# Optimization experiments

Hardware: AMD Instinct MI355X
Metric: run time of the kernel (lower is better)

## Reference

```python
import jax, jax.numpy as jnp
import numpy as np

C = 768
NUM_HEADS = 12
HEAD_DIM = C // NUM_HEADS
AGENT_NUM = 49
POOL = 7  # sqrt(agent_num)
EPS = 1e-5


def _with_bias_ln(x, w, b):
    # LayerNorm over last dim, biased variance, eps=1e-5
    mu = x.mean(-1, keepdims=True)
    var = ((x - mu) ** 2).mean(-1, keepdims=True)
    return (x - mu) / jnp.sqrt(var + EPS) * w + b


def setup_inputs() -> dict:
    key = jax.random.key(0)
    ks = jax.random.split(key, 8)
    B, H, W = 8, 56, 56
    inp = {
        "x": jax.random.normal(ks[0], (B, C, H, W), dtype=jnp.float32),
        "y": jax.random.normal(ks[1], (B, C, H, W), dtype=jnp.float32),
        "ln1_w": jnp.ones((C,), jnp.float32),
        "ln1_b": jnp.zeros((C,), jnp.float32),
        "ln2_w": jnp.ones((C,), jnp.float32),
        "ln2_b": jnp.zeros((C,), jnp.float32),
        # torch nn.Linear weight layout: [out, in]
        "wq1": jax.random.normal(ks[2], (C, C), jnp.float32) * 0.02,
        "wq2": jax.random.normal(ks[3], (C, C), jnp.float32) * 0.02,
        "wkv": jax.random.normal(ks[4], (2 * C, C), jnp.float32) * 0.02,
        "wproj": jax.random.normal(ks[5], (C, C), jnp.float32) * 0.02,
        "bproj": jnp.zeros((C,), jnp.float32),
    }
    return inp


def reference(x, y, ln1_w, ln1_b, ln2_w, ln2_b, wq1, wq2, wkv, wproj, bproj):
    b, c, h, w = x.shape
    n = h * w
    nh, hd = NUM_HEADS, HEAD_DIM
    scale = hd ** (-0.5)

    # NCHW -> (b, n, c) token layout
    xt = x.reshape(b, c, n).transpose(0, 2, 1)
    yt = y.reshape(b, c, n).transpose(0, 2, 1)

    xt = _with_bias_ln(xt, ln1_w, ln1_b)
    yt = _with_bias_ln(yt, ln2_w, ln2_b)

    q = jnp.einsum('bnc,oc->bno', xt, wq1)        # (b, n, c)
    q_agent = jnp.einsum('bnc,oc->bno', yt, wq2)  # (b, n, c)
    kv = jnp.einsum('bnc,oc->bno', xt, wkv)       # (b, n, 2c)
    k, v = kv[..., :c], kv[..., c:]

    # Adaptive avg pool q_agent to 7x7 agent tokens (56/7 = 8 exact windows)
    qa = q_agent.reshape(b, h, w, c)
    qa = qa.reshape(b, POOL, h // POOL, POOL, w // POOL, c).mean(axis=(2, 4))
    agent_tokens = qa.reshape(b, AGENT_NUM, c)

    # split heads: (b, heads, tokens, head_dim)
    q = q.reshape(b, n, nh, hd).transpose(0, 2, 1, 3)
    k = k.reshape(b, n, nh, hd).transpose(0, 2, 1, 3)
    v = v.reshape(b, n, nh, hd).transpose(0, 2, 1, 3)
    at = agent_tokens.reshape(b, AGENT_NUM, nh, hd).transpose(0, 2, 1, 3)

    # stage 1: agent tokens attend over keys -> pooled values
    agent_attn = jax.nn.softmax(jnp.einsum('bhad,bhnd->bhan', at * scale, k), axis=-1)
    agent_v = jnp.einsum('bhan,bhnd->bhad', agent_attn, v)  # (b, h, A, hd)

    # stage 2: queries attend over agent tokens
    q_attn = jax.nn.softmax(jnp.einsum('bhnd,bhad->bhna', q * scale, at), axis=-1)
    out = jnp.einsum('bhna,bhad->bhnd', q_attn, agent_v)  # (b, h, n, hd)

    out = out.transpose(0, 2, 1, 3).reshape(b, n, c)
    out = jnp.einsum('bnc,oc->bno', out, wproj) + bproj
    return out.transpose(0, 2, 1).reshape(b, c, h, w)
```

## Files before the change

### kernel.cpp

```cpp
#include <hip/hip_runtime.h>

typedef unsigned short u16;
typedef u16 u16x4 __attribute__((ext_vector_type(4)));
typedef u16 u16x8 __attribute__((ext_vector_type(8)));
typedef __bf16 bf16x8 __attribute__((ext_vector_type(8)));
typedef float f32x4 __attribute__((ext_vector_type(4)));

__device__ __forceinline__ float b2f(u16 u) {
    union { unsigned int i; float f; } v; v.i = ((unsigned int)u) << 16; return v.f;
}
__device__ __forceinline__ u16 f2b(float f) {
    union { float f; unsigned int i; } v; v.f = f;
    unsigned int r = v.i + 0x7fffu + ((v.i >> 16) & 1u);
    return (u16)(r >> 16);
}
__device__ __forceinline__ void gload_lds16(const u16* g, u16* l) {
    __builtin_amdgcn_global_load_lds(
        (const __attribute__((address_space(1))) void*)g,
        (__attribute__((address_space(3))) void*)l, 16, 0, 0);
}
__device__ __forceinline__ bf16x8 ones_frag() {
    union { u16x8 u; bf16x8 b; } v;
    #pragma unroll
    for (int i = 0; i < 8; ++i) v.u[i] = 0x3F80;
    return v.b;
}
#define LGKM_BARRIER do { \
    asm volatile("s_waitcnt lgkmcnt(0)" ::: "memory"); \
    __builtin_amdgcn_s_barrier(); \
    __builtin_amdgcn_sched_barrier(0); } while (0)

__global__ __launch_bounds__(256) void pack_w_kernel(
    const float* __restrict__ wq1, const float* __restrict__ wq2,
    const float* __restrict__ wkv, const float* __restrict__ wproj,
    u16* __restrict__ wcat, u16* __restrict__ wq2b, u16* __restrict__ wpb,
    u16* __restrict__ at_a) {
    int e = blockIdx.x * 256 + threadIdx.x;
    const float scale = 0.125f;
    wcat[e]           = f2b(wq1[e] * scale);
    wcat[589824 + e]  = f2b(wkv[e] * scale);
    wcat[1179648 + e] = f2b(wkv[589824 + e]);
    wq2b[e]           = f2b(wq2[e]);
    wpb[e]            = f2b(wproj[e]);
    if (e < 92160) {
        int bb = e / 11520, rem = e - bb * 11520;
        at_a[(size_t)bb * 49152 + 37632 + rem] = 0;
    }
}

__global__ __launch_bounds__(256) void xstats_kernel(
    const float* __restrict__ x, float* __restrict__ xmu, float* __restrict__ xrs) {
    __shared__ float red[16][64];
    __shared__ float red2[16][64];
    const int bx = blockIdx.x;
    const int b = bx / 49, tile = bx - b * 49;
    const int pos0 = tile * 64;
    const int t = threadIdx.x, pq = t & 15, q = t >> 4;
    const float* xb = x + (size_t)b * 2408448 + pos0;
    f32x4 s = {0.f, 0.f, 0.f, 0.f}, s2 = {0.f, 0.f, 0.f, 0.f};
    #pragma unroll 8
    for (int c = q; c < 768; c += 16) {
        f32x4 v = *(const f32x4*)&xb[(size_t)c * 3136 + pq * 4];
        s += v; s2 += v * v;
    }
    *(f32x4*)&red[q][pq * 4] = s;
    *(f32x4*)&red2[q][pq * 4] = s2;
    __syncthreads();
    if (t < 64) {
        float ss = 0.f, qq = 0.f;
        #pragma unroll
        for (int r = 0; r < 16; ++r) { ss += red[r][t]; qq += red2[r][t]; }
        float mu = ss * (1.0f / 768.0f);
        float var = qq * (1.0f / 768.0f) - mu * mu;
        xmu[(size_t)b * 3136 + pos0 + t] = mu;
        xrs[(size_t)b * 3136 + pos0 + t] = rsqrtf(var + 1e-5f);
    }
}

__global__ __launch_bounds__(256) void xnorm_kernel(
    const float* __restrict__ x, const float* __restrict__ lw,
    const float* __restrict__ lb, const float* __restrict__ xmu,
    const float* __restrict__ xrs, u16* __restrict__ xn) {
    __shared__ u16 tl[128][68];
    const int bx = blockIdx.x;
    const int half = blockIdx.y;
    const int b = bx / 49, tile = bx - b * 49;
    const int pos0 = tile * 64;
    const int t = threadIdx.x;
    const int pq = t & 15, q = t >> 4;
    const int p = t >> 2, sub = t & 3;
    const float* xb = x + (size_t)b * 2408448 + pos0;
    const float mu = xmu[(size_t)b * 3136 + pos0 + p];
    const float rs = xrs[(size_t)b * 3136 + pos0 + p];
    const size_t orow = ((size_t)(b * 3136 + pos0 + p)) * 768;
    for (int ci = 0; ci < 3; ++ci) {
        const int c0 = half * 384 + ci * 128;
        #pragma unroll
        for (int s8 = 0; s8 < 8; ++s8) {
            const int cr = s8 * 16 + q;
            f32x4 v = *(const f32x4*)&xb[(size_t)(c0 + cr) * 3136 + pq * 4];
            u16x4 pk;
            pk[0] = f2b(v[0]); pk[1] = f2b(v[1]); pk[2] = f2b(v[2]); pk[3] = f2b(v[3]);
            *(u16x4*)&tl[cr][pq * 4] = pk;
        }
        __syncthreads();
        #pragma unroll
        for (int k = 0; k < 4; ++k) {
            const int cb = k * 32 + sub * 8;
            f32x4 w0 = *(const f32x4*)&lw[c0 + cb];
            f32x4 w1 = *(const f32x4*)&lw[c0 + cb + 4];
            f32x4 b0 = *(const f32x4*)&lb[c0 + cb];
            f32x4 b1 = *(const f32x4*)&lb[c0 + cb + 4];
            u16x8 o;
            #pragma unroll
            for (int j = 0; j < 4; ++j) {
                float v = b2f(tl[cb + j][p]);
                o[j] = f2b((v - mu) * rs * w0[j] + b0[j]);
            }
            #pragma unroll
            for (int j = 0; j < 4; ++j) {
                float v = b2f(tl[cb + 4 + j][p]);
                o[4 + j] = f2b((v - mu) * rs * w1[j] + b1[j]);
            }
            *(u16x8*)&xn[orow + c0 + cb] = o;
        }
        __syncthreads();
    }
}

__global__ __launch_bounds__(256) void y_stats_kernel(
    const float* __restrict__ y, float* __restrict__ rsb, float* __restrict__ mrsb) {
    __shared__ float red[16][64];
    __shared__ float red2[16][64];
    const int bx = blockIdx.x;
    const int b = bx / 49, tile = bx - b * 49;
    const int pos0 = tile * 64;
    const int t = threadIdx.x, pq = t & 15, q = t >> 4;
    const float* yb = y + (size_t)b * 2408448 + pos0;
    f32x4 s = {0.f, 0.f, 0.f, 0.f}, s2 = {0.f, 0.f, 0.f, 0.f};
    #pragma unroll 8
    for (int c = q; c < 768; c += 16) {
        f32x4 v = *(const f32x4*)&yb[(size_t)c * 3136 + pq * 4];
        s += v; s2 += v * v;
    }
    *(f32x4*)&red[q][pq * 4] = s;
    *(f32x4*)&red2[q][pq * 4] = s2;
    __syncthreads();
    if (t < 64) {
        float ss = 0.f, qq = 0.f;
        #pragma unroll
        for (int r = 0; r < 16; ++r) { ss += red[r][t]; qq += red2[r][t]; }
        float mu = ss * (1.0f / 768.0f);
        float var = qq * (1.0f / 768.0f) - mu * mu;
        float rv = rsqrtf(var + 1e-5f);
        rsb[(size_t)b * 3136 + pos0 + t] = rv;
        mrsb[(size_t)b * 3136 + pos0 + t] = mu * rv;
    }
}

__global__ __launch_bounds__(256) void y_pool_kernel(
    const float* __restrict__ y, const float* __restrict__ lw,
    const float* __restrict__ lb, const float* __restrict__ rsb,
    const float* __restrict__ mrsb, u16* __restrict__ at_a) {
    const int cgrp = blockIdx.x;
    const int bpi  = blockIdx.y;
    const int b = bpi / 7, pi = bpi - b * 7;
    const int t = threadIdx.x, lane = t & 63, w = t >> 6;
    const int pbase = b * 3136 + pi * 448;
    const int p0 = (lane >> 3) * 56 + (lane & 7);
    float rsv[7], s3f[7];
    #pragma unroll
    for (int it = 0; it < 7; ++it) {
        rsv[it] = rsb[pbase + p0 + it * 8];
        float m = mrsb[pbase + p0 + it * 8];
        #pragma unroll
        for (int msk = 1; msk < 64; msk <<= 1) m += __shfl_xor(m, msk, 64);
        s3f[it] = m;
    }
    const float* yb = y + (size_t)b * 2408448 + pi * 448 + p0;
    u16* yo = at_a + ((size_t)b * 64 + pi * 7) * 768;
    for (int ci = 0; ci < 16; ++ci) {
        const int c = cgrp * 64 + w * 16 + ci;
        const float* yc = yb + (size_t)c * 3136;
        float v[7];
        #pragma unroll
        for (int it = 0; it < 7; ++it) v[it] = yc[it * 8] * rsv[it];
        #pragma unroll
        for (int it = 0; it < 7; ++it) {
            float s = v[it];
            #pragma unroll
            for (int msk = 1; msk < 64; msk <<= 1) s += __shfl_xor(s, msk, 64);
            v[it] = s;
        }
        if (lane == 0) {
            const float wv = lw[c], bv = lb[c];
            #pragma unroll
            for (int it = 0; it < 7; ++it)
                yo[(size_t)it * 768 + c] = f2b(wv * (v[it] - s3f[it]) * (1.0f / 64.0f) + bv);
        }
    }
}

template<int MODE, int NCT>
__global__ __launch_bounds__(256) void gemm_bt_kernel(
    const u16* __restrict__ A, const u16* __restrict__ B,
    u16* __restrict__ qk, u16* __restrict__ vT,
    float* __restrict__ Cf, const float* __restrict__ bias) {
    __shared__ u16 As[128 * 64];
    __shared__ u16 Bs[128 * 64];
    const int t = threadIdx.x;
    const int lane = t & 63;
    const int w = t >> 6;
    const int wr = w >> 1, wc = w & 1;
    const int l15 = lane & 15, l4 = lane >> 4;

    const int nwg = gridDim.x;
    const int orig = blockIdx.x;
    const int xcd = orig & 7;
    const int qd = nwg >> 3, r = nwg & 7;
    const int wg = (xcd < r ? xcd * (qd + 1) : r * (qd + 1) + (xcd - r) * qd) + (orig >> 3);
    const int ct = wg % NCT, rt = wg / NCT;

    const u16* Ab = A + (size_t)rt * 128 * 768;
    const u16* Bb = B + (size_t)ct * 128 * 768;
    const int grh = lane >> 3;
    const int gsl = (lane & 7) ^ grh;

    f32x4 acc[4][4];
    #pragma unroll
    for (int mi = 0; mi < 4; ++mi)
        #pragma unroll
        for (int ni = 0; ni < 4; ++ni)
            acc[mi][ni] = (f32x4){0.f, 0.f, 0.f, 0.f};

    for (int kt = 0; kt < 12; ++kt) {
        if (kt) __syncthreads();
        #pragma unroll
        for (int i = 0; i < 4; ++i) {
            const int chunk = w * 4 + i;
            const int row = chunk * 8 + grh;
            gload_lds16(Ab + (size_t)row * 768 + kt * 64 + gsl * 8, &As[chunk * 512]);
            gload_lds16(Bb + (size_t)row * 768 + kt * 64 + gsl * 8, &Bs[chunk * 512]);
        }
        __syncthreads();
        #pragma unroll
        for (int ks = 0; ks < 2; ++ks) {
            bf16x8 af[4], bfv[4];
            #pragma unroll
            for (int mi = 0; mi < 4; ++mi) {
                const int row = wr * 64 + mi * 16 + l15;
                af[mi] = *(const bf16x8*)&As[row * 64 + (((ks * 4 + l4) ^ (row & 7)) * 8)];
            }
            #pragma unroll
            for (int ni = 0; ni < 4; ++ni) {
                const int row = wc * 64 + ni * 16 + l15;
                bfv[ni] = *(const bf16x8*)&Bs[row * 64 + (((ks * 4 + l4) ^ (row & 7)) * 8)];
            }
            #pragma unroll
            for (int mi = 0; mi < 4; ++mi)
                #pragma unroll
                for (int ni = 0; ni < 4; ++ni)
                    acc[mi][ni] = __builtin_amdgcn_mfma_f32_16x16x32_bf16(
                        af[mi], bfv[ni], acc[mi][ni], 0, 0, 0);
        }
    }

    if constexpr (MODE == 0) {
        #pragma unroll
        for (int mi = 0; mi < 4; ++mi)
            #pragma unroll
            for (int ni = 0; ni < 4; ++ni) {
                const int row0 = rt * 128 + wr * 64 + mi * 16 + l4 * 4;
                const int col = ct * 128 + wc * 64 + ni * 16 + l15;
                if (col < 1536) {
                    #pragma unroll
                    for (int rr = 0; rr < 4; ++rr)
                        qk[(size_t)(row0 + rr) * 1536 + col] = f2b(acc[mi][ni][rr]);
                } else {
                    const int c = col - 1536;
                    const int bb = row0 / 3136;
                    const int nn2 = row0 - bb * 3136;
                    u16x4 pk;
                    #pragma unroll
                    for (int rr = 0; rr < 4; ++rr) pk[rr] = f2b(acc[mi][ni][rr]);
                    *(u16x4*)&vT[((size_t)(bb * 768 + c)) * 3136 + nn2] = pk;
                }
            }
    } else if constexpr (MODE == 1) {
        #pragma unroll
        for (int ni = 0; ni < 4; ++ni) {
            const int col = ct * 128 + wc * 64 + ni * 16 + l15;
            const float bv = bias[col];
            #pragma unroll
            for (int mi = 0; mi < 4; ++mi) {
                const int grow = rt * 128 + wr * 64 + mi * 16 + l4 * 4;
                const int bb = grow / 3136;
                const int nn2 = grow - bb * 3136;
                f32x4 vv = acc[mi][ni];
                vv[0] += bv; vv[1] += bv; vv[2] += bv; vv[3] += bv;
                *(f32x4*)(Cf + (size_t)bb * 2408448 + (size_t)col * 3136 + nn2) = vv;
            }
        }
    } else {
        #pragma unroll
        for (int mi = 0; mi < 4; ++mi)
            #pragma unroll
            for (int ni = 0; ni < 4; ++ni) {
                const int row0 = rt * 128 + wr * 64 + mi * 16 + l4 * 4;
                const int col = ct * 128 + wc * 64 + ni * 16 + l15;
                #pragma unroll
                for (int rr = 0; rr < 4; ++rr)
                    qk[(size_t)(row0 + rr) * 768 + col] = f2b(acc[mi][ni][rr]);
            }
    }
}

__global__ __launch_bounds__(256) void agent_attn_kernel(
    const u16* __restrict__ at_bf, const u16* __restrict__ qk,
    const u16* __restrict__ vT, float* __restrict__ ps,
    float* __restrict__ pav_t) {
    __shared__ u16 k_lds[2][64 * 64];
    __shared__ u16 vt_lds[2][64 * 64];
    __shared__ u16 p_lds[64 * 64];
    const int ns = blockIdx.x;
    const int bh = blockIdx.y;
    const int b = bh / 12, h = bh - b * 12;
    const int t = threadIdx.x, lane = t & 63, w = t >> 6;
    const int l15 = lane & 15, l4 = lane >> 4;

    bf16x8 atf[2];
    #pragma unroll
    for (int ks = 0; ks < 2; ++ks)
        atf[ks] = *(const bf16x8*)&at_bf[((size_t)b * 64 + 16 * w + l15) * 768 + h * 64 + ks * 32 + l4 * 8];
    const bf16x8 onef = ones_frag();

    f32x4 acc_o[4], acc_den[4];
    #pragma unroll
    for (int mi = 0; mi < 4; ++mi) {
        acc_o[mi] = (f32x4){0.f, 0.f, 0.f, 0.f};
        acc_den[mi] = (f32x4){0.f, 0.f, 0.f, 0.f};
    }

    auto STAGE = [&](int buf, int tile) {
        const int n0 = ns * 448 + tile * 64;
        #pragma unroll
        for (int p = 0; p < 2; ++p) {
            const int row = p * 32 + w * 8 + (lane >> 3);
            const int sc = ((lane & 7) ^ (row & 7)) * 8;
            gload_lds16(qk + ((size_t)(b * 3136 + n0 + row)) * 1536 + 768 + h * 64 + sc,
                        &k_lds[buf][(p * 32 + w * 8) * 64]);
            gload_lds16(vT + ((size_t)(bh * 64 + row)) * 3136 + n0 + sc,
                        &vt_lds[buf][(p * 32 + w * 8) * 64]);
        }
    };

    STAGE(0, 0);
    for (int tile = 0; tile < 7; ++tile) {
        const int buf = tile & 1;
        __syncthreads();
        if (tile < 6) STAGE(buf ^ 1, tile + 1);
        f32x4 acc_s[4];
        #pragma unroll
        for (int mi = 0; mi < 4; ++mi) acc_s[mi] = (f32x4){0.f, 0.f, 0.f, 0.f};
        __builtin_amdgcn_s_setprio(1);
        #pragma unroll
        for (int ks = 0; ks < 2; ++ks)
            #pragma unroll
            for (int mi = 0; mi < 4; ++mi) {
                const int row = 16 * mi + l15;
                bf16x8 kf = *(const bf16x8*)&k_lds[buf][row * 64 + (((ks * 4 + l4) ^ (row & 7)) * 8)];
                acc_s[mi] = __builtin_amdgcn_mfma_f32_16x16x32_bf16(kf, atf[ks], acc_s[mi], 0, 0, 0);
            }
        __builtin_amdgcn_s_setprio(0);
        const int a_w = 16 * w + l15;
        #pragma unroll
        for (int mi = 0; mi < 4; ++mi) {
            u16x4 pk;
            #pragma unroll
            for (int rr = 0; rr < 4; ++rr) pk[rr] = f2b(__expf(acc_s[mi][rr]));
            const int pp = (2 * mi + (l4 >> 1)) ^ (a_w & 7);
            *(u16x4*)((char*)p_lds + a_w * 128 + pp * 16 + (l4 & 1) * 8) = pk;
        }
        LGKM_BARRIER;
        __builtin_amdgcn_s_setprio(1);
        #pragma unroll
        for (int ks = 0; ks < 2; ++ks) {
            const int d = 16 * w + l15;
            bf16x8 vf = *(const bf16x8*)&vt_lds[buf][d * 64 + (((ks * 4 + l4) ^ (d & 7)) * 8)];
            #pragma unroll
            for (int mi = 0; mi < 4; ++mi) {
                const int a = 16 * mi + l15;
                bf16x8 pf = *(const bf16x8*)((char*)p_lds + a * 128 + (((ks * 4 + l4) ^ (a & 7)) * 16));
                acc_o[mi] = __builtin_amdgcn_mfma_f32_16x16x32_bf16(pf, vf, acc_o[mi], 0, 0, 0);
                acc_den[mi] = __builtin_amdgcn_mfma_f32_16x16x32_bf16(onef, pf, acc_den[mi], 0, 0, 0);
            }
        }
        __builtin_amdgcn_s_setprio(0);
    }
    const size_t pbase = (size_t)bh * 7 + ns;
    if (w == 0 && lane < 16) {
        #pragma unroll
        for (int mi = 0; mi < 4; ++mi)
            ps[pbase * 64 + 16 * mi + lane] = acc_den[mi][0];
    }
    #pragma unroll
    for (int mi = 0; mi < 4; ++mi)
        *(f32x4*)&pav_t[(pbase * 64 + 16 * w + l15) * 64 + 16 * mi + l4 * 4] = acc_o[mi];
}

__global__ __launch_bounds__(256) void combine_kernel(
    const float* __restrict__ ps, const float* __restrict__ pav_t,
    u16* __restrict__ av_t) {
    __shared__ float sinv[64];
    const int bh = blockIdx.x;
    const int t = threadIdx.x;
    if (t < 64) {
        float s = 0.f;
        #pragma unroll
        for (int ns = 0; ns < 7; ++ns) s += ps[((size_t)bh * 7 + ns) * 64 + t];
        sinv[t] = 1.0f / s;
    }
    __syncthreads();
    const int d = t >> 2, aseg = t & 3;
    f32x4 acc[4];
    #pragma unroll
    for (int g = 0; g < 4; ++g) acc[g] = (f32x4){0.f, 0.f, 0.f, 0.f};
    #pragma unroll
    for (int ns = 0; ns < 7; ++ns) {
        const float* src = pav_t + (((size_t)bh * 7 + ns) * 64 + d) * 64 + aseg * 16;
        #pragma unroll
        for (int g = 0; g < 4; ++g) acc[g] += *(const f32x4*)&src[g * 4];
    }
    u16x8 o0, o1;
    #pragma unroll
    for (int g = 0; g < 4; ++g)
        #pragma unroll
        for (int j = 0; j < 4; ++j) {
            const u16 v = f2b(acc[g][j] * sinv[aseg * 16 + g * 4 + j]);
            if (g < 2) o0[g * 4 + j] = v; else o1[(g - 2) * 4 + j] = v;
        }
    u16* dst = av_t + ((size_t)bh * 64 + d) * 64 + aseg * 16;
    *(u16x8*)dst = o0;
    *(u16x8*)(dst + 8) = o1;
}

__global__ __launch_bounds__(256) void q_attn_kernel(
    const u16* __restrict__ at_bf, const u16* __restrict__ qk,
    const u16* __restrict__ av_t, u16* __restrict__ attn_out) {
    __shared__ u16 q_lds[2][64 * 64];
    __shared__ u16 p_lds[64 * 64];
    const int grp = blockIdx.x;
    const int bh = blockIdx.y;
    const int b = bh / 12, h = bh - b * 12;
    const int t = threadIdx.x, lane = t & 63, w = t >> 6;
    const int l15 = lane & 15, l4 = lane >> 4;

    bf16x8 atf[4][2], avf[4][2];
    #pragma unroll
    for (int mi = 0; mi < 4; ++mi)
        #pragma unroll
        for (int ks = 0; ks < 2; ++ks) {
            atf[mi][ks] = *(const bf16x8*)&at_bf[((size_t)b * 64 + 16 * mi + l15) * 768 + h * 64 + ks * 32 + l4 * 8];
            avf[mi][ks] = *(const bf16x8*)&av_t[((size_t)bh * 64 + 16 * mi + l15) * 64 + ks * 32 + l4 * 8];
        }
    const bf16x8 onef = ones_frag();

    auto STAGE_Q = [&](int buf, int nt) {
        const int n0 = nt * 64;
        #pragma unroll
        for (int p = 0; p < 2; ++p) {
            const int row = p * 32 + w * 8 + (lane >> 3);
            const int sc = ((lane & 7) ^ (row & 7)) * 8;
            gload_lds16(qk + ((size_t)(b * 3136 + n0 + row)) * 1536 + h * 64 + sc,
                        &q_lds[buf][(p * 32 + w * 8) * 64]);
        }
    };

    STAGE_Q(0, grp * 7);
    const int nn = 16 * w + l15;
    for (int i = 0; i < 7; ++i) {
        const int buf = i & 1;
        const int nt = grp * 7 + i;
        __syncthreads();
        if (i < 6) STAGE_Q(buf ^ 1, nt + 1);
        f32x4 acc_l[4];
        #pragma unroll
        for (int mi = 0; mi < 4; ++mi) acc_l[mi] = (f32x4){0.f, 0.f, 0.f, 0.f};
        __builtin_amdgcn_s_setprio(1);
        #pragma unroll
        for (int ks = 0; ks < 2; ++ks) {
            bf16x8 qf = *(const bf16x8*)&q_lds[buf][nn * 64 + (((ks * 4 + l4) ^ (nn & 7)) * 8)];
            #pragma unroll
            for (int mi = 0; mi < 4; ++mi)
                acc_l[mi] = __builtin_amdgcn_mfma_f32_16x16x32_bf16(atf[mi][ks], qf, acc_l[mi], 0, 0, 0);
        }
        __builtin_amdgcn_s_setprio(0);
        #pragma unroll
        for (int mi = 0; mi < 4; ++mi) {
            u16x4 pk;
            #pragma unroll
            for (int rr = 0; rr < 4; ++rr) {
                const int a = 16 * mi + l4 * 4 + rr;
                pk[rr] = (a < 49) ? f2b(__expf(acc_l[mi][rr])) : (u16)0;
            }
            const int pp = (2 * mi + (l4 >> 1)) ^ (nn & 7);
            *(u16x4*)((char*)p_lds + nn * 128 + pp * 16 + (l4 & 1) * 8) = pk;
        }
        LGKM_BARRIER;
        f32x4 acc_o[4], den;
        #pragma unroll
        for (int mi = 0; mi < 4; ++mi) acc_o[mi] = (f32x4){0.f, 0.f, 0.f, 0.f};
        den = (f32x4){0.f, 0.f, 0.f, 0.f};
        __builtin_amdgcn_s_setprio(1);
        #pragma unroll
        for (int ks = 0; ks < 2; ++ks) {
            bf16x8 pf = *(const bf16x8*)((char*)p_lds + nn * 128 + (((ks * 4 + l4) ^ (nn & 7)) * 16));
            den = __builtin_amdgcn_mfma_f32_16x16x32_bf16(onef, pf, den, 0, 0, 0);
            #pragma unroll
            for (int mi = 0; mi < 4; ++mi)
                acc_o[mi] = __builtin_amdgcn_mfma_f32_16x16x32_bf16(avf[mi][ks], pf, acc_o[mi], 0, 0, 0);
        }
        __builtin_amdgcn_s_setprio(0);
        const float rinv = 1.0f / den[0];
        const size_t obase = ((size_t)(b * 3136 + nt * 64 + nn)) * 768 + h * 64;
        #pragma unroll
        for (int mi = 0; mi < 4; ++mi) {
            u16x4 ov;
            #pragma unroll
            for (int rr = 0; rr < 4; ++rr) ov[rr] = f2b(acc_o[mi][rr] * rinv);
            *(u16x4*)&attn_out[obase + 16 * mi + l4 * 4] = ov;
        }
    }
}

extern "C" void kernel_launch(void* const* d_in, const int* in_sizes, int n_in,
                              void* d_out, int out_size, void* d_ws, size_t ws_size,
                              hipStream_t stream) {
    (void)in_sizes; (void)n_in; (void)out_size; (void)ws_size;
    const float* x     = (const float*)d_in[0];
    const float* y     = (const float*)d_in[1];
    const float* ln1w  = (const float*)d_in[2];
    const float* ln1b  = (const float*)d_in[3];
    const float* ln2w  = (const float*)d_in[4];
    const float* ln2b  = (const float*)d_in[5];
    const float* wq1   = (const float*)d_in[6];
    const float* wq2   = (const float*)d_in[7];
    const float* wkv   = (const float*)d_in[8];
    const float* wproj = (const float*)d_in[9];
    const float* bproj = (const float*)d_in[10];
    float* out = (float*)d_out;

    char* ws = (char*)d_ws;
    u16*   xn     = (u16*)(ws);
    u16*   qk     = (u16*)(ws + 38535168);
    u16*   vT     = (u16*)(ws + 115605504);
    u16*   wcat   = (u16*)(ws + 154140672);
    u16*   wq2b   = (u16*)(ws + 157679616);
    u16*   wpb    = (u16*)(ws + 158859264);
    u16*   at_a   = (u16*)(ws + 160038912);
    u16*   at_bf  = (u16*)(ws + 160825344);
    float* ps     = (float*)(ws + 161611776);
    float* rsb    = (float*)(ws + 161783808);
    float* mrsb   = (float*)(ws + 161884160);
    u16*   av_t   = (u16*)(ws + 161984512);
    float* xmu    = (float*)(ws + 162770944);
    float* xrs    = (float*)(ws + 162871296);
    float* pav_t  = (float*)(ws);
    u16*   attn_out = xn;

    pack_w_kernel<<<dim3(2304), dim3(256), 0, stream>>>(wq1, wq2, wkv, wproj, wcat, wq2b, wpb, at_a);
    xstats_kernel<<<dim3(392), dim3(256), 0, stream>>>(x, xmu, xrs);
    xnorm_kernel<<<dim3(392, 2), dim3(256), 0, stream>>>(x, ln1w, ln1b, xmu, xrs, xn);
    y_stats_kernel<<<dim3(392), dim3(256), 0, stream>>>(y, rsb, mrsb);
    y_pool_kernel<<<dim3(12, 56), dim3(256), 0, stream>>>(y, ln2w, ln2b, rsb, mrsb, at_a);
    gemm_bt_kernel<0, 18><<<dim3(3528), dim3(256), 0, stream>>>(xn, wcat, qk, vT, nullptr, nullptr);
    gemm_bt_kernel<2, 6><<<dim3(24), dim3(256), 0, stream>>>(at_a, wq2b, at_bf, nullptr, nullptr, nullptr);
    agent_attn_kernel<<<dim3(7, 96), dim3(256), 0, stream>>>(at_bf, qk, vT, ps, pav_t);
    combine_kernel<<<dim3(96), dim3(256), 0, stream>>>(ps, pav_t, av_t);
    q_attn_kernel<<<dim3(7, 96), dim3(256), 0, stream>>>(at_bf, qk, av_t, attn_out);
    gemm_bt_kernel<1, 6><<<dim3(1176), dim3(256), 0, stream>>>(attn_out, wpb, nullptr, nullptr, out, bproj);
}
```

Baseline: 320.5 us.

## Use two-wave GEMM tiles, merge x/y stats kernels, drop setprio hints

The GEMM kernel now runs with 128 threads (two waves), and each wave computes a 64x128 output slab with 32 accumulators instead of four waves each holding 64x64. The goal is more MFMA work per LDS fragment load and fewer waves per block, at the cost of higher register pressure and possibly lower occupancy. The x and y LayerNorm statistics kernels are merged into one 784-block launch to save a launch and improve fill. The s_setprio hints are removed from the attention kernels.

```diff
diff --git a/kernel.cpp b/kernel.cpp
--- a/kernel.cpp
+++ b/kernel.cpp
@@ -48,19 +48,23 @@
     }
 }
 
-__global__ __launch_bounds__(256) void xstats_kernel(
-    const float* __restrict__ x, float* __restrict__ xmu, float* __restrict__ xrs) {
+__global__ __launch_bounds__(256) void xy_stats_kernel(
+    const float* __restrict__ x, const float* __restrict__ y,
+    float* __restrict__ xmu, float* __restrict__ xrs,
+    float* __restrict__ rsb, float* __restrict__ mrsb) {
     __shared__ float red[16][64];
     __shared__ float red2[16][64];
-    const int bx = blockIdx.x;
+    const int bx0 = blockIdx.x;
+    const int isY = bx0 >= 392;
+    const int bx = isY ? bx0 - 392 : bx0;
     const int b = bx / 49, tile = bx - b * 49;
     const int pos0 = tile * 64;
     const int t = threadIdx.x, pq = t & 15, q = t >> 4;
-    const float* xb = x + (size_t)b * 2408448 + pos0;
+    const float* src = (isY ? y : x) + (size_t)b * 2408448 + pos0;
     f32x4 s = {0.f, 0.f, 0.f, 0.f}, s2 = {0.f, 0.f, 0.f, 0.f};
     #pragma unroll 8
     for (int c = q; c < 768; c += 16) {
-        f32x4 v = *(const f32x4*)&xb[(size_t)c * 3136 + pq * 4];
+        f32x4 v = *(const f32x4*)&src[(size_t)c * 3136 + pq * 4];
         s += v; s2 += v * v;
     }
     *(f32x4*)&red[q][pq * 4] = s;
@@ -72,8 +76,10 @@
         for (int r = 0; r < 16; ++r) { ss += red[r][t]; qq += red2[r][t]; }
         float mu = ss * (1.0f / 768.0f);
         float var = qq * (1.0f / 768.0f) - mu * mu;
-        xmu[(size_t)b * 3136 + pos0 + t] = mu;
-        xrs[(size_t)b * 3136 + pos0 + t] = rsqrtf(var + 1e-5f);
+        float rv = rsqrtf(var + 1e-5f);
+        const size_t o = (size_t)b * 3136 + pos0 + t;
+        if (isY) { rsb[o] = rv; mrsb[o] = mu * rv; }
+        else     { xmu[o] = mu; xrs[o] = rv; }
     }
 }
 
@@ -128,36 +134,6 @@
     }
 }
 
-__global__ __launch_bounds__(256) void y_stats_kernel(
-    const float* __restrict__ y, float* __restrict__ rsb, float* __restrict__ mrsb) {
-    __shared__ float red[16][64];
-    __shared__ float red2[16][64];
-    const int bx = blockIdx.x;
-    const int b = bx / 49, tile = bx - b * 49;
-    const int pos0 = tile * 64;
-    const int t = threadIdx.x, pq = t & 15, q = t >> 4;
-    const float* yb = y + (size_t)b * 2408448 + pos0;
-    f32x4 s = {0.f, 0.f, 0.f, 0.f}, s2 = {0.f, 0.f, 0.f, 0.f};
-    #pragma unroll 8
-    for (int c = q; c < 768; c += 16) {
-        f32x4 v = *(const f32x4*)&yb[(size_t)c * 3136 + pq * 4];
-        s += v; s2 += v * v;
-    }
-    *(f32x4*)&red[q][pq * 4] = s;
-    *(f32x4*)&red2[q][pq * 4] = s2;
-    __syncthreads();
-    if (t < 64) {
-        float ss = 0.f, qq = 0.f;
-        #pragma unroll
-        for (int r = 0; r < 16; ++r) { ss += red[r][t]; qq += red2[r][t]; }
-        float mu = ss * (1.0f / 768.0f);
-        float var = qq * (1.0f / 768.0f) - mu * mu;
-        float rv = rsqrtf(var + 1e-5f);
-        rsb[(size_t)b * 3136 + pos0 + t] = rv;
-        mrsb[(size_t)b * 3136 + pos0 + t] = mu * rv;
-    }
-}
-
 __global__ __launch_bounds__(256) void y_pool_kernel(
     const float* __restrict__ y, const float* __restrict__ lw,
     const float* __restrict__ lb, const float* __restrict__ rsb,
@@ -202,7 +178,7 @@
 }
 
 template<int MODE, int NCT>
-__global__ __launch_bounds__(256) void gemm_bt_kernel(
+__global__ __launch_bounds__(128) void gemm2w_kernel(
     const u16* __restrict__ A, const u16* __restrict__ B,
     u16* __restrict__ qk, u16* __restrict__ vT,
     float* __restrict__ Cf, const float* __restrict__ bias) {
@@ -211,7 +187,6 @@
     const int t = threadIdx.x;
     const int lane = t & 63;
     const int w = t >> 6;
-    const int wr = w >> 1, wc = w & 1;
     const int l15 = lane & 15, l4 = lane >> 4;
 
     const int nwg = gridDim.x;
@@ -226,18 +201,18 @@
     const int grh = lane >> 3;
     const int gsl = (lane & 7) ^ grh;
 
-    f32x4 acc[4][4];
+    f32x4 acc[4][8];
     #pragma unroll
     for (int mi = 0; mi < 4; ++mi)
         #pragma unroll
-        for (int ni = 0; ni < 4; ++ni)
+        for (int ni = 0; ni < 8; ++ni)
             acc[mi][ni] = (f32x4){0.f, 0.f, 0.f, 0.f};
 
     for (int kt = 0; kt < 12; ++kt) {
         if (kt) __syncthreads();
         #pragma unroll
-        for (int i = 0; i < 4; ++i) {
-            const int chunk = w * 4 + i;
+        for (int i = 0; i < 8; ++i) {
+            const int chunk = w * 8 + i;
             const int row = chunk * 8 + grh;
             gload_lds16(Ab + (size_t)row * 768 + kt * 64 + gsl * 8, &As[chunk * 512]);
             gload_lds16(Bb + (size_t)row * 768 + kt * 64 + gsl * 8, &Bs[chunk * 512]);
@@ -245,21 +220,21 @@
         __syncthreads();
         #pragma unroll
         for (int ks = 0; ks < 2; ++ks) {
-            bf16x8 af[4], bfv[4];
+            bf16x8 af[4], bfv[8];
             #pragma unroll
             for (int mi = 0; mi < 4; ++mi) {
-                const int row = wr * 64 + mi * 16 + l15;
+                const int row = w * 64 + mi * 16 + l15;
                 af[mi] = *(const bf16x8*)&As[row * 64 + (((ks * 4 + l4) ^ (row & 7)) * 8)];
             }
             #pragma unroll
-            for (int ni = 0; ni < 4; ++ni) {
-                const int row = wc * 64 + ni * 16 + l15;
+            for (int ni = 0; ni < 8; ++ni) {
+                const int row = ni * 16 + l15;
                 bfv[ni] = *(const bf16x8*)&Bs[row * 64 + (((ks * 4 + l4) ^ (row & 7)) * 8)];
             }
             #pragma unroll
             for (int mi = 0; mi < 4; ++mi)
                 #pragma unroll
-                for (int ni = 0; ni < 4; ++ni)
+                for (int ni = 0; ni < 8; ++ni)
                     acc[mi][ni] = __builtin_amdgcn_mfma_f32_16x16x32_bf16(
                         af[mi], bfv[ni], acc[mi][ni], 0, 0, 0);
         }
@@ -269,9 +244,9 @@
         #pragma unroll
         for (int mi = 0; mi < 4; ++mi)
             #pragma unroll
-            for (int ni = 0; ni < 4; ++ni) {
-                const int row0 = rt * 128 + wr * 64 + mi * 16 + l4 * 4;
-                const int col = ct * 128 + wc * 64 + ni * 16 + l15;
+            for (int ni = 0; ni < 8; ++ni) {
+                const int row0 = rt * 128 + w * 64 + mi * 16 + l4 * 4;
+                const int col = ct * 128 + ni * 16 + l15;
                 if (col < 1536) {
                     #pragma unroll
                     for (int rr = 0; rr < 4; ++rr)
@@ -288,12 +263,12 @@
             }
     } else if constexpr (MODE == 1) {
         #pragma unroll
-        for (int ni = 0; ni < 4; ++ni) {
-            const int col = ct * 128 + wc * 64 + ni * 16 + l15;
+        for (int ni = 0; ni < 8; ++ni) {
+            const int col = ct * 128 + ni * 16 + l15;
             const float bv = bias[col];
             #pragma unroll
             for (int mi = 0; mi < 4; ++mi) {
-                const int grow = rt * 128 + wr * 64 + mi * 16 + l4 * 4;
+                const int grow = rt * 128 + w * 64 + mi * 16 + l4 * 4;
                 const int bb = grow / 3136;
                 const int nn2 = grow - bb * 3136;
                 f32x4 vv = acc[mi][ni];
@@ -305,9 +280,9 @@
         #pragma unroll
         for (int mi = 0; mi < 4; ++mi)
             #pragma unroll
-            for (int ni = 0; ni < 4; ++ni) {
-                const int row0 = rt * 128 + wr * 64 + mi * 16 + l4 * 4;
-                const int col = ct * 128 + wc * 64 + ni * 16 + l15;
+            for (int ni = 0; ni < 8; ++ni) {
+                const int row0 = rt * 128 + w * 64 + mi * 16 + l4 * 4;
+                const int col = ct * 128 + ni * 16 + l15;
                 #pragma unroll
                 for (int rr = 0; rr < 4; ++rr)
                     qk[(size_t)(row0 + rr) * 768 + col] = f2b(acc[mi][ni][rr]);
@@ -362,7 +337,6 @@
         f32x4 acc_s[4];
         #pragma unroll
         for (int mi = 0; mi < 4; ++mi) acc_s[mi] = (f32x4){0.f, 0.f, 0.f, 0.f};
-        __builtin_amdgcn_s_setprio(1);
         #pragma unroll
         for (int ks = 0; ks < 2; ++ks)
             #pragma unroll
@@ -371,7 +345,6 @@
                 bf16x8 kf = *(const bf16x8*)&k_lds[buf][row * 64 + (((ks * 4 + l4) ^ (row & 7)) * 8)];
                 acc_s[mi] = __builtin_amdgcn_mfma_f32_16x16x32_bf16(kf, atf[ks], acc_s[mi], 0, 0, 0);
             }
-        __builtin_amdgcn_s_setprio(0);
         const int a_w = 16 * w + l15;
         #pragma unroll
         for (int mi = 0; mi < 4; ++mi) {
@@ -382,7 +355,6 @@
             *(u16x4*)((char*)p_lds + a_w * 128 + pp * 16 + (l4 & 1) * 8) = pk;
         }
         LGKM_BARRIER;
-        __builtin_amdgcn_s_setprio(1);
         #pragma unroll
         for (int ks = 0; ks < 2; ++ks) {
             const int d = 16 * w + l15;
@@ -395,7 +367,6 @@
                 acc_den[mi] = __builtin_amdgcn_mfma_f32_16x16x32_bf16(onef, pf, acc_den[mi], 0, 0, 0);
             }
         }
-        __builtin_amdgcn_s_setprio(0);
     }
     const size_t pbase = (size_t)bh * 7 + ns;
     if (w == 0 && lane < 16) {
@@ -486,7 +457,6 @@
         f32x4 acc_l[4];
         #pragma unroll
         for (int mi = 0; mi < 4; ++mi) acc_l[mi] = (f32x4){0.f, 0.f, 0.f, 0.f};
-        __builtin_amdgcn_s_setprio(1);
         #pragma unroll
         for (int ks = 0; ks < 2; ++ks) {
             bf16x8 qf = *(const bf16x8*)&q_lds[buf][nn * 64 + (((ks * 4 + l4) ^ (nn & 7)) * 8)];
@@ -494,7 +464,6 @@
             for (int mi = 0; mi < 4; ++mi)
                 acc_l[mi] = __builtin_amdgcn_mfma_f32_16x16x32_bf16(atf[mi][ks], qf, acc_l[mi], 0, 0, 0);
         }
-        __builtin_amdgcn_s_setprio(0);
         #pragma unroll
         for (int mi = 0; mi < 4; ++mi) {
             u16x4 pk;
@@ -511,7 +480,6 @@
         #pragma unroll
         for (int mi = 0; mi < 4; ++mi) acc_o[mi] = (f32x4){0.f, 0.f, 0.f, 0.f};
         den = (f32x4){0.f, 0.f, 0.f, 0.f};
-        __builtin_amdgcn_s_setprio(1);
         #pragma unroll
         for (int ks = 0; ks < 2; ++ks) {
             bf16x8 pf = *(const bf16x8*)((char*)p_lds + nn * 128 + (((ks * 4 + l4) ^ (nn & 7)) * 16));
@@ -520,7 +488,6 @@
             for (int mi = 0; mi < 4; ++mi)
                 acc_o[mi] = __builtin_amdgcn_mfma_f32_16x16x32_bf16(avf[mi][ks], pf, acc_o[mi], 0, 0, 0);
         }
-        __builtin_amdgcn_s_setprio(0);
         const float rinv = 1.0f / den[0];
         const size_t obase = ((size_t)(b * 3136 + nt * 64 + nn)) * 768 + h * 64;
         #pragma unroll
@@ -569,14 +536,13 @@
     u16*   attn_out = xn;
 
     pack_w_kernel<<<dim3(2304), dim3(256), 0, stream>>>(wq1, wq2, wkv, wproj, wcat, wq2b, wpb, at_a);
-    xstats_kernel<<<dim3(392), dim3(256), 0, stream>>>(x, xmu, xrs);
+    xy_stats_kernel<<<dim3(784), dim3(256), 0, stream>>>(x, y, xmu, xrs, rsb, mrsb);
     xnorm_kernel<<<dim3(392, 2), dim3(256), 0, stream>>>(x, ln1w, ln1b, xmu, xrs, xn);
-    y_stats_kernel<<<dim3(392), dim3(256), 0, stream>>>(y, rsb, mrsb);
     y_pool_kernel<<<dim3(12, 56), dim3(256), 0, stream>>>(y, ln2w, ln2b, rsb, mrsb, at_a);
-    gemm_bt_kernel<0, 18><<<dim3(3528), dim3(256), 0, stream>>>(xn, wcat, qk, vT, nullptr, nullptr);
-    gemm_bt_kernel<2, 6><<<dim3(24), dim3(256), 0, stream>>>(at_a, wq2b, at_bf, nullptr, nullptr, nullptr);
+    gemm2w_kernel<0, 18><<<dim3(3528), dim3(128), 0, stream>>>(xn, wcat, qk, vT, nullptr, nullptr);
+    gemm2w_kernel<2, 6><<<dim3(24), dim3(128), 0, stream>>>(at_a, wq2b, at_bf, nullptr, nullptr, nullptr);
     agent_attn_kernel<<<dim3(7, 96), dim3(256), 0, stream>>>(at_bf, qk, vT, ps, pav_t);
     combine_kernel<<<dim3(96), dim3(256), 0, stream>>>(ps, pav_t, av_t);
     q_attn_kernel<<<dim3(7, 96), dim3(256), 0, stream>>>(at_bf, qk, av_t, attn_out);
-    gemm_bt_kernel<1, 6><<<dim3(1176), dim3(256), 0, stream>>>(attn_out, wpb, nullptr, nullptr, out, bproj);
-}
+    gemm2w_kernel<1, 6><<<dim3(1176), dim3(128), 0, stream>>>(attn_out, wpb, nullptr, nullptr, out, bproj);
+}
```

Result: slower. 366.0 us (+14.2%).
